# Kernel optimization log

Hardware: AMD Instinct MI355X
Metric: run time of the kernel (lower is better)

## Reference

```python
import jax, jax.numpy as jnp
import numpy as np

N_STATE = 2048
N_HEAD = 16
HEAD_DIM = N_STATE // N_HEAD  # 128
ROPE_THETA = 10000.0


def setup_inputs() -> dict:
    key = jax.random.key(0)
    ks = jax.random.split(key, 8)
    B, S, D = 2, 2048, N_STATE
    scale = 1.0 / np.sqrt(D)
    x = jax.random.normal(ks[0], (B, S, D), dtype=jnp.float32)
    Wq = jax.random.normal(ks[1], (D, D), dtype=jnp.float32) * scale
    bq = jnp.zeros((D,), dtype=jnp.float32)
    Wk = jax.random.normal(ks[2], (D, D), dtype=jnp.float32) * scale  # key has no bias
    Wv = jax.random.normal(ks[3], (D, D), dtype=jnp.float32) * scale
    bv = jnp.zeros((D,), dtype=jnp.float32)
    Wo = jax.random.normal(ks[4], (D, D), dtype=jnp.float32) * scale
    bo = jnp.zeros((D,), dtype=jnp.float32)
    return {"x": x, "Wq": Wq, "bq": bq, "Wk": Wk, "Wv": Wv, "bv": bv, "Wo": Wo, "bo": bo}


def _rope(t, pos):
    # t: [B, S, H, hd]; torchtune-style interleaved rotary (pairs of adjacent dims)
    hd = t.shape[-1]
    inv_freq = 1.0 / (ROPE_THETA ** (jnp.arange(0, hd, 2, dtype=jnp.float32) / hd))  # [hd/2]
    ang = pos[:, None] * inv_freq[None, :]                    # [S, hd/2]
    cos = jnp.cos(ang)[None, :, None, :].astype(t.dtype)       # [1,S,1,hd/2]
    sin = jnp.sin(ang)[None, :, None, :].astype(t.dtype)
    t1 = t[..., 0::2]
    t2 = t[..., 1::2]
    rot = jnp.stack([t1 * cos - t2 * sin, t2 * cos + t1 * sin], axis=-1)
    return rot.reshape(t.shape)


def reference(x, Wq, bq, Wk, Wv, bv, Wo, bo):
    B, S, D = x.shape
    H, hd = N_HEAD, D // N_HEAD
    q = (x @ Wq.T + bq).reshape(B, S, H, hd)
    k = (x @ Wk.T).reshape(B, S, H, hd)
    v = (x @ Wv.T + bv).reshape(B, S, H, hd)
    pos = jnp.arange(S, dtype=jnp.float32)
    q = _rope(q, pos)
    k = _rope(k, pos)
    # [B,H,S,hd]
    q = q.transpose(0, 2, 1, 3)
    k = k.transpose(0, 2, 1, 3)
    v = v.transpose(0, 2, 1, 3)
    scale = 1.0 / jnp.sqrt(jnp.asarray(hd, dtype=x.dtype))
    scores = jnp.einsum('bhqd,bhkd->bhqk', q, k) * scale       # [B,H,S,S]
    causal = jnp.tril(jnp.ones((S, S), dtype=bool))
    scores = jnp.where(causal[None, None], scores, jnp.finfo(scores.dtype).min)
    probs = jax.nn.softmax(scores, axis=-1)
    a = jnp.einsum('bhqk,bhkd->bhqd', probs, v)                # [B,H,S,hd]
    a = a.transpose(0, 2, 1, 3).reshape(B, S, D)
    return a @ Wo.T + bo
```

## Files before the change

### kernel.cpp

```cpp
#include <hip/hip_runtime.h>
#include <stdint.h>

typedef float f32x4 __attribute__((ext_vector_type(4)));
typedef __bf16 bf16x8 __attribute__((ext_vector_type(8)));
typedef unsigned short us8 __attribute__((ext_vector_type(8)));
typedef unsigned short us4 __attribute__((ext_vector_type(4)));
typedef unsigned int u32;

#define MFMA16(A, B, C) __builtin_amdgcn_mfma_f32_16x16x32_bf16( \
    __builtin_bit_cast(bf16x8, (A)), __builtin_bit_cast(bf16x8, (B)), (C), 0, 0, 0)

__device__ __forceinline__ unsigned short f2bf(float f) {
  u32 u = __builtin_bit_cast(u32, f);
  u = u + 0x7fffu + ((u >> 16) & 1u);
  return (unsigned short)(u >> 16);
}
__device__ __forceinline__ float bf2f(unsigned short b) {
  u32 u = ((u32)b) << 16;
  return __builtin_bit_cast(float, u);
}
__device__ __forceinline__ void gload16(const void* g, void* lds) {
  __builtin_amdgcn_global_load_lds((const __attribute__((address_space(1))) u32*)g,
                                   (__attribute__((address_space(3))) u32*)lds, 16, 0, 0);
}

__global__ __launch_bounds__(256) void convert_all(
    const float* __restrict__ x, const float* __restrict__ wq, const float* __restrict__ wk,
    const float* __restrict__ wv, const float* __restrict__ wo,
    unsigned short* __restrict__ xb, unsigned short* __restrict__ wcat,
    unsigned short* __restrict__ wob) {
  int tid = blockIdx.x * 256 + threadIdx.x;
  int nth = gridDim.x * 256;
  const float* srcs[5] = {x, wq, wk, wv, wo};
  unsigned short* dsts[5] = {xb, wcat, wcat + 4194304, wcat + 8388608, wob};
  const int n4s[5] = {2097152, 1048576, 1048576, 1048576, 1048576};
#pragma unroll
  for (int sg = 0; sg < 5; ++sg) {
    const float4* s = (const float4*)srcs[sg];
    us4* d = (us4*)dsts[sg];
    int n4 = n4s[sg];
    for (int i = tid; i < n4; i += nth) {
      float4 v = s[i];
      us4 o;
      o[0] = f2bf(v.x); o[1] = f2bf(v.y); o[2] = f2bf(v.z); o[3] = f2bf(v.w);
      d[i] = o;
    }
  }
}

template <int EPI>
__global__ __launch_bounds__(512, 2) void gemmsw(
    const unsigned short* __restrict__ A, const unsigned short* __restrict__ B,
    int nTN, int N,
    float* __restrict__ outF, const float* __restrict__ bias,
    unsigned short* __restrict__ qb, unsigned short* __restrict__ kb,
    unsigned short* __restrict__ vtb, const float* __restrict__ bq,
    const float* __restrict__ bv) {
  constexpr int KT = 32;
  __shared__ alignas(16) char L[131072];
  char* Lp = L;
  int bid = (int)blockIdx.x, nwg = (int)gridDim.x;
  {
    int qq = nwg >> 3;
    int xcd = bid & 7, idx = bid >> 3;
    bid = xcd * qq + idx;
  }
  int tm = bid / nTN, tn = bid % nTN;
  int t = (int)threadIdx.x, l = t & 63, w = t >> 6;
  int g = l >> 4, ln = l & 15;
  int wr = w >> 2, wc = w & 3;
  int lr = l >> 3, lc = l & 7;
  int scol = lc ^ lr;
  const unsigned short* pAs = A + (size_t)(tm * 256 + w * 8 + lr) * 2048 + scol * 8;
  const unsigned short* pBs = B + (size_t)(tn * 256 + w * 8 + lr) * 2048 + scol * 8;

  f32x4 acc[2][2][4][2] = {};
  us8 af[4][2], bf[2][2][2];

#define FENCE asm volatile("" ::: "memory")
#define BAR do { FENCE; __builtin_amdgcn_s_barrier(); FENCE; } while (0)
#define VMW_(n) asm volatile("s_waitcnt vmcnt(" #n ")" ::: "memory")
#define VMW(n) VMW_(n)
#define STA(i, kt, bufsel) do { if ((kt) < KT)                                \
    gload16(pAs + (size_t)(i) * 131072 + (size_t)(kt) * 64,                   \
            Lp + (bufsel) * 65536 + (i) * 8192 + w * 1024); } while (0)
#define STB(i, kt, bufsel) do { if ((kt) < KT)                                \
    gload16(pBs + (size_t)(i) * 131072 + (size_t)(kt) * 64,                   \
            Lp + (bufsel) * 65536 + 32768 + (i) * 8192 + w * 1024); } while (0)
#define RD_A(mh_, bufsel) do {                                                \
    _Pragma("unroll") for (int mf = 0; mf < 4; ++mf)                          \
    _Pragma("unroll") for (int kc = 0; kc < 2; ++kc)                          \
      af[mf][kc] = *(const us8*)(Lp + (bufsel) * 65536 +                      \
          (wr * 128 + (mh_) * 64 + mf * 16 + ln) * 128 +                      \
          ((kc * 64 + g * 16) ^ ((ln & 7) << 4)));                            \
  } while (0)
#define RD_B(nh_, bufsel) do {                                                \
    _Pragma("unroll") for (int nf = 0; nf < 2; ++nf)                          \
    _Pragma("unroll") for (int kc = 0; kc < 2; ++kc)                          \
      bf[nh_][nf][kc] = *(const us8*)(Lp + (bufsel) * 65536 + 32768 +         \
          (wc * 64 + (nh_) * 32 + nf * 16 + ln) * 128 +                       \
          ((kc * 64 + g * 16) ^ ((ln & 7) << 4)));                            \
  } while (0)
#define MM(mh_, nh_) do {                                                     \
    __builtin_amdgcn_s_setprio(1);                                            \
    _Pragma("unroll") for (int mf = 0; mf < 4; ++mf)                          \
    _Pragma("unroll") for (int nf = 0; nf < 2; ++nf)                          \
    _Pragma("unroll") for (int kc = 0; kc < 2; ++kc)                          \
      acc[mh_][nh_][mf][nf] = MFMA16(af[mf][kc], bf[nh_][nf][kc],             \
                                     acc[mh_][nh_][mf][nf]);                  \
    __builtin_amdgcn_s_setprio(0);                                            \
  } while (0)
#define TILE(kt, b, VM1, VM3) do {                                            \
   RD_A(0, b); RD_B(0, b); RD_B(1, b);                                 \
          STB(0, (kt) + 1, (b) ^ 1); STB(1, (kt) + 1, (b) ^ 1);               \
          BAR; MM(0, 0); BAR;                                                 \
   STB(2, (kt) + 1, (b) ^ 1); STB(3, (kt) + 1, (b) ^ 1);               \
          BAR; MM(0, 1); VMW(VM1); BAR;                                       \
   RD_A(1, b);                                                         \
          STA(0, (kt) + 1, (b) ^ 1); STA(2, (kt) + 1, (b) ^ 1);               \
          BAR; MM(1, 0); BAR;                                                 \
   STA(1, (kt) + 1, (b) ^ 1); STA(3, (kt) + 1, (b) ^ 1);               \
          MM(1, 1); VMW(VM3); BAR;                                            \
} while (0)

  STB(0, 0, 0); STB(1, 0, 0); STB(2, 0, 0); STB(3, 0, 0);
  STA(0, 0, 0); STA(2, 0, 0); STA(1, 0, 0); STA(3, 0, 0);
  VMW(0); BAR;

#pragma unroll 1
  for (int kt = 0; kt < 30; kt += 2) {
    TILE(kt, 0, 4, 2);
    TILE(kt + 1, 1, 4, 2);
  }
  TILE(30, 0, 4, 2);
  TILE(31, 1, 0, 0);

#undef TILE
#undef MM
#undef RD_B
#undef RD_A
#undef STB
#undef STA
#undef VMW
#undef VMW_
#undef BAR
#undef FENCE

  if (EPI == 1) {
#pragma unroll
    for (int mh = 0; mh < 2; ++mh)
#pragma unroll
    for (int nh = 0; nh < 2; ++nh)
#pragma unroll
    for (int mf = 0; mf < 4; ++mf)
#pragma unroll
    for (int nf = 0; nf < 2; ++nf) {
      int n = tn * 256 + wc * 64 + nh * 32 + nf * 16 + ln;
      float bz = bias[n];
      int m0 = tm * 256 + wr * 128 + mh * 64 + mf * 16 + g * 4;
#pragma unroll
      for (int r = 0; r < 4; ++r)
        outF[(size_t)(m0 + r) * N + n] = acc[mh][nh][mf][nf][r] + bz;
    }
  } else {
#pragma unroll
    for (int mh = 0; mh < 2; ++mh)
#pragma unroll
    for (int nh = 0; nh < 2; ++nh)
#pragma unroll
    for (int mf = 0; mf < 4; ++mf)
#pragma unroll
    for (int nf = 0; nf < 2; ++nf) {
      int n6 = tn * 256 + wc * 64 + nh * 32 + nf * 16 + ln;
      int sel = n6 >> 11, d = n6 & 2047, h = d >> 7, hd = d & 127;
      int m0 = tm * 256 + wr * 128 + mh * 64 + mf * 16 + g * 4;
      int b = m0 >> 11, s0 = m0 & 2047;
      if (sel == 2) {
        float badd = bv[d];
        us4 pk;
#pragma unroll
        for (int r = 0; r < 4; ++r) pk[r] = f2bf(acc[mh][nh][mf][nf][r] + badd);
        *(us4*)&vtb[((size_t)(b * 16 + h) * 128 + hd) * 2048 + s0] = pk;
      } else {
        unsigned short* dst = sel ? kb : qb;
        float badd = sel ? 0.f : bq[d];
#pragma unroll
        for (int r = 0; r < 4; ++r)
          dst[((size_t)(b * 16 + h) * 2048 + (s0 + r)) * 128 + hd] =
              f2bf(acc[mh][nh][mf][nf][r] + badd);
      }
    }
  }
}

template <int EPI>
__global__ __launch_bounds__(512, 2) void gemm2(
    const unsigned short* __restrict__ A, const unsigned short* __restrict__ B,
    int nTN, int N,
    float* __restrict__ outF, const float* __restrict__ bias) {
  constexpr int K = 2048, KT = 64;
  __shared__ alignas(16) char L[4 * 24576];
  int bid = (int)blockIdx.x, nwg = (int)gridDim.x;
  {
    int qq = nwg >> 3;
    int xcd = bid & 7, idx = bid >> 3;
    bid = xcd * qq + idx;
  }
  int tm = bid / nTN, tn = bid % nTN;
  int t = (int)threadIdx.x, l = t & 63, w = t >> 6;
  int g = l >> 4, ln = l & 15;
  int wr = w >> 2, wc = w & 3;
  const unsigned short* Ab =
      A + (size_t)(tm * 128 + w * 16 + (l >> 2)) * K + (l & 3) * 8;
  const unsigned short* Bb =
      B + (size_t)(tn * 256 + w * 16 + (l >> 2)) * K + (l & 3) * 8;
  f32x4 acc[4][4] = {};

#define STAGE(tile) do {                                                      \
    char* Lb = L + ((tile) & 3) * 24576 + w * 1024;                           \
    int kc = (tile) * 32;                                                     \
    gload16(Ab + kc, Lb);                                                     \
    gload16(Bb + kc, Lb + 8192);                                              \
    gload16(Bb + (size_t)128 * K + kc, Lb + 16384);                           \
  } while (0)

#define GITER(kt, VM) do {                                                    \
    asm volatile("s_waitcnt vmcnt(" #VM ")" ::: "memory");                    \
    __builtin_amdgcn_s_barrier();                                             \
    __builtin_amdgcn_sched_barrier(0);                                        \
    asm volatile("" ::: "memory");                                            \
    if ((kt) + 3 < KT) STAGE((kt) + 3);                                       \
    const unsigned short* Lc = (const unsigned short*)(L + ((kt) & 3) * 24576); \
    us8 af[4], bfr[4];                                                        \
    _Pragma("unroll") for (int mf = 0; mf < 4; ++mf)                          \
      af[mf] = *(const us8*)&Lc[(wr * 64 + mf * 16 + ln) * 32 + g * 8];       \
    _Pragma("unroll") for (int nf = 0; nf < 4; ++nf)                          \
      bfr[nf] = *(const us8*)&Lc[4096 + (wc * 64 + nf * 16 + ln) * 32 + g * 8]; \
    __builtin_amdgcn_s_setprio(1);                                            \
    _Pragma("unroll") for (int mf = 0; mf < 4; ++mf)                          \
      _Pragma("unroll") for (int nf = 0; nf < 4; ++nf)                        \
        acc[mf][nf] = MFMA16(af[mf], bfr[nf], acc[mf][nf]);                   \
    __builtin_amdgcn_s_setprio(0);                                            \
  } while (0)

  STAGE(0); STAGE(1); STAGE(2);
#pragma unroll 1
  for (int kt = 0; kt < KT - 2; ++kt) GITER(kt, 6);
  GITER(KT - 2, 3);
  GITER(KT - 1, 0);
#undef STAGE
#undef GITER

#pragma unroll
  for (int mf = 0; mf < 4; ++mf)
#pragma unroll
    for (int nf = 0; nf < 4; ++nf) {
      int n = tn * 256 + wc * 64 + nf * 16 + ln;
      float bz = bias[n];
#pragma unroll
      for (int r = 0; r < 4; ++r) {
        int m = tm * 128 + wr * 64 + mf * 16 + g * 4 + r;
        outF[(size_t)m * N + n] = acc[mf][nf][r] + bz;
      }
    }
}

__global__ __launch_bounds__(256) void rope_k(u32* __restrict__ q, u32* __restrict__ k) {
  int idx = blockIdx.x * 256 + threadIdx.x;
  int i = idx & 63;
  int s = (idx >> 6) & 2047;
  float ang = (float)s * exp2f(-(float)i * 0.2076205059304703f);
  float sv, cv;
  sincosf(ang, &sv, &cv);
  u32 qu = q[idx];
  float a0 = bf2f((unsigned short)(qu & 0xffff)), a1 = bf2f((unsigned short)(qu >> 16));
  q[idx] = (u32)f2bf(a0 * cv - a1 * sv) | ((u32)f2bf(a1 * cv + a0 * sv) << 16);
  u32 ku = k[idx];
  float b0 = bf2f((unsigned short)(ku & 0xffff)), b1 = bf2f((unsigned short)(ku >> 16));
  k[idx] = (u32)f2bf(b0 * cv - b1 * sv) | ((u32)f2bf(b1 * cv + b0 * sv) << 16);
}

__global__ __launch_bounds__(512) void attn_k(
    const unsigned short* __restrict__ qg, const unsigned short* __restrict__ kg,
    const unsigned short* __restrict__ vtg, unsigned short* __restrict__ ab) {
  __shared__ alignas(16) unsigned short Kl[64 * 128];
  __shared__ alignas(16) unsigned short Vl[128 * 64];
  __shared__ alignas(16) unsigned short Pl[8][16 * 72];
  int bh = (int)blockIdx.x & 31;
  int pr = (int)blockIdx.x >> 5;
  int t = (int)threadIdx.x, l = t & 63, w = t >> 6;
  int g = l >> 4, ln = l & 15;
  int b = bh >> 4, h = bh & 15;
  const size_t bq0 = (size_t)bh * 2048 * 128;

#pragma unroll 1
  for (int half = 0; half < 2; ++half) {
    int qt = half ? 15 - pr : pr;
    int qbase = qt * 128;
    int qrow = qbase + w * 16 + ln;
    us8 qf[4];
#pragma unroll
    for (int kf = 0; kf < 4; ++kf)
      qf[kf] = *(const us8*)&qg[bq0 + (size_t)qrow * 128 + kf * 32 + g * 8];
    f32x4 o[8] = {};
    float mrow = -1e30f, lrow = 0.f;
    int nkt = (qbase >> 6) + 2;
#pragma unroll 1
    for (int kt = 0; kt < nkt; ++kt) {
      __syncthreads();
#pragma unroll
      for (int i = 0; i < 2; ++i) {
        int fb = i * 8192 + w * 1024;
        int flat = fb + l * 16;
        int row = flat >> 8, colb = flat & 255;
        int sc = colb ^ ((row & 7) << 4);
        gload16(kg + (bq0 + (size_t)(kt * 64 + row) * 128 + (sc >> 1)), (char*)Kl + fb);
        int rv = flat >> 7, cv2 = flat & 127;
        int scv = cv2 ^ ((rv & 7) << 4);
        gload16(vtg + (bq0 + (size_t)rv * 2048 + kt * 64 + (scv >> 1)), (char*)Vl + fb);
      }
      __syncthreads();
      f32x4 st[4];
#pragma unroll
      for (int kfr = 0; kfr < 4; ++kfr) {
        f32x4 acc = {};
        int row = kfr * 16 + ln;
        int swz = (row & 7) << 4;
#pragma unroll
        for (int kf = 0; kf < 4; ++kf) {
          us8 kfrag = *(const us8*)((const char*)Kl + row * 256 + ((kf * 64 + g * 16) ^ swz));
          acc = MFMA16(kfrag, qf[kf], acc);
        }
        st[kfr] = acc;
      }
      float pmax = -1e30f;
#pragma unroll
      for (int kfr = 0; kfr < 4; ++kfr)
#pragma unroll
        for (int r = 0; r < 4; ++r) {
          int key = kt * 64 + kfr * 16 + g * 4 + r;
          float sv = key <= qrow ? st[kfr][r] * 0.08838834764831845f : -1e30f;
          st[kfr][r] = sv;
          pmax = fmaxf(pmax, sv);
        }
      pmax = fmaxf(pmax, __shfl_xor(pmax, 16));
      pmax = fmaxf(pmax, __shfl_xor(pmax, 32));
      if (__ballot(pmax > mrow + 8.f)) {
        float mnew = pmax > mrow + 8.f ? pmax : mrow;
        float corr = exp2f((mrow - mnew) * 1.44269504f);
        mrow = mnew;
        lrow *= corr;
#pragma unroll
        for (int r = 0; r < 4; ++r) {
          float cr = __shfl(corr, g * 4 + r);
#pragma unroll
          for (int nf = 0; nf < 8; ++nf) o[nf][r] *= cr;
        }
      }
      float lsum = 0.f;
#pragma unroll
      for (int kfr = 0; kfr < 4; ++kfr) {
        us4 pk;
#pragma unroll
        for (int r = 0; r < 4; ++r) {
          float p = exp2f((st[kfr][r] - mrow) * 1.44269504f);
          lsum += p;
          pk[r] = f2bf(p);
        }
        *(us4*)&Pl[w][ln * 72 + kfr * 16 + g * 4] = pk;
      }
      lsum += __shfl_xor(lsum, 16);
      lsum += __shfl_xor(lsum, 32);
      lrow += lsum;
#pragma unroll
      for (int kf2 = 0; kf2 < 2; ++kf2) {
        us8 pa = *(const us8*)&Pl[w][ln * 72 + kf2 * 32 + g * 8];
#pragma unroll
        for (int nf = 0; nf < 8; ++nf) {
          int row = nf * 16 + ln;
          us8 vb = *(const us8*)((const char*)Vl + row * 128 +
                                 ((kf2 * 64 + g * 16) ^ ((row & 7) << 4)));
          o[nf] = MFMA16(pa, vb, o[nf]);
        }
      }
    }
    float invl = 1.f / lrow;
#pragma unroll
    for (int r = 0; r < 4; ++r) {
      float ir = __shfl(invl, g * 4 + r);
      int srow = qbase + w * 16 + g * 4 + r;
      size_t base = ((size_t)b * 2048 + srow) * 2048 + h * 128 + ln;
#pragma unroll
      for (int nf = 0; nf < 8; ++nf) ab[base + (size_t)nf * 16] = f2bf(o[nf][r] * ir);
    }
  }
}

extern "C" void kernel_launch(void* const* d_in, const int* in_sizes, int n_in,
                              void* d_out, int out_size, void* d_ws, size_t ws_size,
                              hipStream_t stream) {
  const float* x  = (const float*)d_in[0];
  const float* Wq = (const float*)d_in[1];
  const float* bq = (const float*)d_in[2];
  const float* Wk = (const float*)d_in[3];
  const float* Wv = (const float*)d_in[4];
  const float* bv = (const float*)d_in[5];
  const float* Wo = (const float*)d_in[6];
  const float* bo = (const float*)d_in[7];
  float* out = (float*)d_out;

  unsigned short* ws = (unsigned short*)d_ws;
  unsigned short* xb   = ws;
  unsigned short* wcat = xb + 8388608;
  unsigned short* wob  = wcat + 12582912;
  unsigned short* qb   = wob + 4194304;
  unsigned short* kb   = qb + 8388608;
  unsigned short* vtb  = kb + 8388608;

  convert_all<<<2048, 256, 0, stream>>>(x, Wq, Wk, Wv, Wo, xb, wcat, wob);
  gemmsw<0><<<384, 512, 0, stream>>>(xb, wcat, 24, 6144,
                                     nullptr, nullptr, qb, kb, vtb, bq, bv);
  rope_k<<<16384, 256, 0, stream>>>((u32*)qb, (u32*)kb);
  attn_k<<<256, 512, 0, stream>>>(qb, kb, vtb, xb );
  gemm2<1><<<256, 512, 0, stream>>>(xb, wob, 8, 2048, out, bo);
}
```

Baseline: 275.6 us.

## Precompute RoPE table, reorder GEMM staging waits, swizzle gemm2 LDS layout

Adds 64 extra blocks to the convert kernel that fill a cos/sin table, which rope_k then reads instead of calling sincosf per element. In the QKV GEMM, the order of the next-tile LDS stores and B-fragment reads is changed so that a wait sits after each matmul quarter, and the prologue waits for only part of its loads. gemm2 XOR-swizzles the 16-byte chunk position in LDS, both in the global-to-LDS load addresses and in the fragment reads, to reduce bank conflicts. These are three separate tweaks. The table adds an extra workspace buffer and an extra global read in rope.

```diff
diff --git a/kernel.cpp b/kernel.cpp
--- a/kernel.cpp
+++ b/kernel.cpp
@@ -28,9 +28,22 @@
     const float* __restrict__ x, const float* __restrict__ wq, const float* __restrict__ wk,
     const float* __restrict__ wv, const float* __restrict__ wo,
     unsigned short* __restrict__ xb, unsigned short* __restrict__ wcat,
-    unsigned short* __restrict__ wob) {
+    unsigned short* __restrict__ wob, float2* __restrict__ tab) {
+  if (blockIdx.x >= 2048) {
+    int t0 = ((int)blockIdx.x - 2048) * 2048 + (int)threadIdx.x * 8;
+#pragma unroll
+    for (int j = 0; j < 8; ++j) {
+      int idx = t0 + j;
+      int s = idx >> 6, i = idx & 63;
+      float ang = (float)s * exp2f(-(float)i * 0.2076205059304703f);
+      float sv, cv;
+      sincosf(ang, &sv, &cv);
+      tab[idx] = make_float2(cv, sv);
+    }
+    return;
+  }
   int tid = blockIdx.x * 256 + threadIdx.x;
-  int nth = gridDim.x * 256;
+  int nth = 2048 * 256;
   const float* srcs[5] = {x, wq, wk, wv, wo};
   unsigned short* dsts[5] = {xb, wcat, wcat + 4194304, wcat + 8388608, wob};
   const int n4s[5] = {2097152, 1048576, 1048576, 1048576, 1048576};
@@ -110,30 +123,31 @@
                                      acc[mh_][nh_][mf][nf]);                  \
     __builtin_amdgcn_s_setprio(0);                                            \
   } while (0)
-#define TILE(kt, b, VM1, VM3) do {                                            \
-   RD_A(0, b); RD_B(0, b); RD_B(1, b);                                 \
+#define TILE(kt, b, VM0, VM1, VM3) do {                                       \
+   RD_A(0, b); RD_B(0, b);                                             \
           STB(0, (kt) + 1, (b) ^ 1); STB(1, (kt) + 1, (b) ^ 1);               \
-          BAR; MM(0, 0); BAR;                                                 \
-   STB(2, (kt) + 1, (b) ^ 1); STB(3, (kt) + 1, (b) ^ 1);               \
+          BAR; MM(0, 0); VMW(VM0); BAR;                                       \
+   RD_B(1, b);                                                         \
+          STA(0, (kt) + 1, (b) ^ 1); STA(2, (kt) + 1, (b) ^ 1);               \
           BAR; MM(0, 1); VMW(VM1); BAR;                                       \
    RD_A(1, b);                                                         \
-          STA(0, (kt) + 1, (b) ^ 1); STA(2, (kt) + 1, (b) ^ 1);               \
+          STB(2, (kt) + 1, (b) ^ 1); STB(3, (kt) + 1, (b) ^ 1);               \
           BAR; MM(1, 0); BAR;                                                 \
    STA(1, (kt) + 1, (b) ^ 1); STA(3, (kt) + 1, (b) ^ 1);               \
           MM(1, 1); VMW(VM3); BAR;                                            \
 } while (0)
 
-  STB(0, 0, 0); STB(1, 0, 0); STB(2, 0, 0); STB(3, 0, 0);
-  STA(0, 0, 0); STA(2, 0, 0); STA(1, 0, 0); STA(3, 0, 0);
-  VMW(0); BAR;
+  STB(0, 0, 0); STB(1, 0, 0); STA(0, 0, 0); STA(2, 0, 0);
+  STB(2, 0, 0); STB(3, 0, 0); STA(1, 0, 0); STA(3, 0, 0);
+  VMW(4); BAR;
 
 #pragma unroll 1
   for (int kt = 0; kt < 30; kt += 2) {
-    TILE(kt, 0, 4, 2);
-    TILE(kt + 1, 1, 4, 2);
-  }
-  TILE(30, 0, 4, 2);
-  TILE(31, 1, 0, 0);
+    TILE(kt, 0, 4, 4, 4);
+    TILE(kt + 1, 1, 4, 4, 4);
+  }
+  TILE(30, 0, 4, 4, 4);
+  TILE(31, 1, 2, 0, 0);
 
 #undef TILE
 #undef MM
@@ -211,9 +225,9 @@
   int g = l >> 4, ln = l & 15;
   int wr = w >> 2, wc = w & 3;
   const unsigned short* Ab =
-      A + (size_t)(tm * 128 + w * 16 + (l >> 2)) * K + (l & 3) * 8;
+      A + (size_t)(tm * 128 + w * 16 + (l >> 2)) * K + (((l & 3) ^ ((l >> 4) & 3))) * 8;
   const unsigned short* Bb =
-      B + (size_t)(tn * 256 + w * 16 + (l >> 2)) * K + (l & 3) * 8;
+      B + (size_t)(tn * 256 + w * 16 + (l >> 2)) * K + (((l & 3) ^ ((l >> 4) & 3))) * 8;
   f32x4 acc[4][4] = {};
 
 #define STAGE(tile) do {                                                      \
@@ -233,9 +247,11 @@
     const unsigned short* Lc = (const unsigned short*)(L + ((kt) & 3) * 24576); \
     us8 af[4], bfr[4];                                                        \
     _Pragma("unroll") for (int mf = 0; mf < 4; ++mf)                          \
-      af[mf] = *(const us8*)&Lc[(wr * 64 + mf * 16 + ln) * 32 + g * 8];       \
+      af[mf] = *(const us8*)&Lc[(wr * 64 + mf * 16 + ln) * 32 +               \
+                                ((g ^ ((ln >> 2) & 3)) * 8)];                 \
     _Pragma("unroll") for (int nf = 0; nf < 4; ++nf)                          \
-      bfr[nf] = *(const us8*)&Lc[4096 + (wc * 64 + nf * 16 + ln) * 32 + g * 8]; \
+      bfr[nf] = *(const us8*)&Lc[4096 + (wc * 64 + nf * 16 + ln) * 32 +       \
+                                 ((g ^ ((ln >> 2) & 3)) * 8)];                \
     __builtin_amdgcn_s_setprio(1);                                            \
     _Pragma("unroll") for (int mf = 0; mf < 4; ++mf)                          \
       _Pragma("unroll") for (int nf = 0; nf < 4; ++nf)                        \
@@ -265,13 +281,11 @@
     }
 }
 
-__global__ __launch_bounds__(256) void rope_k(u32* __restrict__ q, u32* __restrict__ k) {
+__global__ __launch_bounds__(256) void rope_k(u32* __restrict__ q, u32* __restrict__ k,
+                                              const float2* __restrict__ tab) {
   int idx = blockIdx.x * 256 + threadIdx.x;
-  int i = idx & 63;
-  int s = (idx >> 6) & 2047;
-  float ang = (float)s * exp2f(-(float)i * 0.2076205059304703f);
-  float sv, cv;
-  sincosf(ang, &sv, &cv);
+  float2 cs = tab[idx & 131071];
+  float cv = cs.x, sv = cs.y;
   u32 qu = q[idx];
   float a0 = bf2f((unsigned short)(qu & 0xffff)), a1 = bf2f((unsigned short)(qu >> 16));
   q[idx] = (u32)f2bf(a0 * cv - a1 * sv) | ((u32)f2bf(a1 * cv + a0 * sv) << 16);
@@ -416,11 +430,12 @@
   unsigned short* qb   = wob + 4194304;
   unsigned short* kb   = qb + 8388608;
   unsigned short* vtb  = kb + 8388608;
-
-  convert_all<<<2048, 256, 0, stream>>>(x, Wq, Wk, Wv, Wo, xb, wcat, wob);
+  float2* tab = (float2*)(vtb + 8388608);
+
+  convert_all<<<2112, 256, 0, stream>>>(x, Wq, Wk, Wv, Wo, xb, wcat, wob, tab);
   gemmsw<0><<<384, 512, 0, stream>>>(xb, wcat, 24, 6144,
                                      nullptr, nullptr, qb, kb, vtb, bq, bv);
-  rope_k<<<16384, 256, 0, stream>>>((u32*)qb, (u32*)kb);
+  rope_k<<<16384, 256, 0, stream>>>((u32*)qb, (u32*)kb, tab);
   attn_k<<<256, 512, 0, stream>>>(qb, kb, vtb, xb );
   gemm2<1><<<256, 512, 0, stream>>>(xb, wob, 8, 2048, out, bo);
 }
```

New measurement: 276.0 us. About the same (+0.2%).
